# Kernel optimization log

Measured on AMD Instinct MI355X. Metric: run time of the kernel, lower is better.

## Reference

```python
import jax, jax.numpy as jnp
import numpy as np

N = 20000
E = 320000
H = 16
C = 16
NUM_GRAPHS = 64
NEG_SLOPE = 0.2


def _gat(x, edge_index, W, a_src, a_dst, bias):
    # PyG GATConv, concat=True, shared lin for src/dst, eval mode (no dropout)
    h = (x @ W).reshape(-1, H, C)                       # [N,H,C]
    src, dst = edge_index[0], edge_index[1]
    alpha_src = jnp.sum(h * a_src, axis=-1)             # [N,H]
    alpha_dst = jnp.sum(h * a_dst, axis=-1)             # [N,H]
    alpha = alpha_src[src] + alpha_dst[dst]             # [E,H]
    alpha = jax.nn.leaky_relu(alpha, NEG_SLOPE)
    amax = jax.ops.segment_max(alpha, dst, num_segments=N)
    ex = jnp.exp(alpha - amax[dst])
    denom = jax.ops.segment_sum(ex, dst, num_segments=N)
    attn = ex / jnp.where(denom == 0, 1.0, denom)[dst]  # [E,H]
    msg = h[src] * attn[:, :, None]                     # [E,H,C]
    out = jax.ops.segment_sum(msg, dst, num_segments=N) # [N,H,C]
    return out.reshape(-1, H * C) + bias


def setup_inputs() -> dict:
    key = jax.random.key(0)
    ks = jax.random.split(key, 32)
    d = {}
    d['x'] = jax.random.normal(ks[0], (N, 20), dtype=jnp.float32)
    d['edge_index_ipv6'] = jax.random.randint(ks[1], (2, E), 0, N)
    d['edge_attr_ipv6'] = jax.random.normal(ks[2], (E, 19), dtype=jnp.float32)
    d['edge_index_tsch'] = jax.random.randint(ks[3], (2, E), 0, N)
    d['edge_attr_tsch'] = jax.random.normal(ks[4], (E, 7), dtype=jnp.float32)
    d['batch'] = jnp.sort(jax.random.randint(ks[5], (N,), 0, NUM_GRAPHS))
    s = 0.1
    d['W_i'] = jax.random.normal(ks[6], (20, H * C), dtype=jnp.float32) * s
    d['a_src_i'] = jax.random.normal(ks[7], (H, C), dtype=jnp.float32) * s
    d['a_dst_i'] = jax.random.normal(ks[8], (H, C), dtype=jnp.float32) * s
    d['b_i'] = jnp.zeros((H * C,), dtype=jnp.float32)
    d['W_t'] = jax.random.normal(ks[9], (20, H * C), dtype=jnp.float32) * s
    d['a_src_t'] = jax.random.normal(ks[10], (H, C), dtype=jnp.float32) * s
    d['a_dst_t'] = jax.random.normal(ks[11], (H, C), dtype=jnp.float32) * s
    d['b_t'] = jnp.zeros((H * C,), dtype=jnp.float32)
    d['Wf'] = jax.random.normal(ks[12], (512, 64), dtype=jnp.float32) * s
    d['bf'] = jnp.zeros((64,), dtype=jnp.float32)
    d['W1'] = jax.random.normal(ks[13], (64, 32), dtype=jnp.float32) * s
    d['b1'] = jnp.zeros((32,), dtype=jnp.float32)
    d['W2'] = jax.random.normal(ks[14], (32, 16), dtype=jnp.float32) * s
    d['b2'] = jnp.zeros((16,), dtype=jnp.float32)
    d['W3'] = jax.random.normal(ks[15], (16, 16), dtype=jnp.float32) * s
    d['b3'] = jnp.zeros((16,), dtype=jnp.float32)
    d['Wce'] = jax.random.normal(ks[16], (16, 3), dtype=jnp.float32) * s
    d['bce'] = jnp.zeros((3,), dtype=jnp.float32)
    d['Wcv'] = jax.random.normal(ks[17], (16, 3), dtype=jnp.float32) * s
    d['bcv'] = jnp.zeros((3,), dtype=jnp.float32)
    return d


def reference(x, edge_index_ipv6, edge_attr_ipv6, edge_index_tsch, edge_attr_tsch,
              batch, W_i, a_src_i, a_dst_i, b_i, W_t, a_src_t, a_dst_t, b_t,
              Wf, bf, W1, b1, W2, b2, W3, b3, Wce, bce, Wcv, bcv):
    # edge_attr_* are ignored by GATConv (edge_dim=None in PyG), as in original
    n_ipv6 = _gat(x, edge_index_ipv6, W_i, a_src_i, a_dst_i, b_i)
    n_tsch = _gat(x, edge_index_tsch, W_t, a_src_t, a_dst_t, b_t)
    h = jnp.concatenate([n_ipv6, n_tsch], axis=-1)      # [N,512]
    h = jax.nn.relu(h @ Wf + bf)
    h = jax.nn.relu(h @ W1 + b1)
    h = jax.nn.relu(h @ W2 + b2)
    h = jax.nn.relu(h @ W3 + b3)                        # [N,16]
    ssum = jax.ops.segment_sum(h, batch, num_segments=NUM_GRAPHS)
    cnt = jax.ops.segment_sum(jnp.ones((h.shape[0], 1), h.dtype), batch,
                              num_segments=NUM_GRAPHS)
    g = ssum / jnp.where(cnt == 0, 1.0, cnt)            # [G,16]
    out_event = g @ Wce + bce
    out_env = g @ Wcv + bcv
    return out_event, out_env
```

## Files before the change

kernel.cpp:

```cpp
#include <hip/hip_runtime.h>
#include <math.h>

#define N_NODES 20000
#define N_EDGES 320000
#define NG 64
#define NEG 0.2f
#define NCHUNK ((N_NODES + 255) / 256)
#define FLAGBIT (1 << 30)

typedef __attribute__((ext_vector_type(8))) short bf16x8;
typedef __attribute__((ext_vector_type(4))) float f32x4;

__device__ __forceinline__ unsigned short f2bf(float f) {
  unsigned int u = __float_as_uint(f);
  return (unsigned short)((u + 0x7fffu + ((u >> 16) & 1u)) >> 16);
}
__device__ __forceinline__ unsigned int pk2bf(float a, float b) {
  return (unsigned int)f2bf(a) | ((unsigned int)f2bf(b) << 16);
}

__global__ __launch_bounds__(256) void k_front(
    const float* __restrict__ x,
    const float* __restrict__ W_i, const float* __restrict__ as_i, const float* __restrict__ ad_i,
    const float* __restrict__ W_t, const float* __restrict__ as_t, const float* __restrict__ ad_t,
    const float* __restrict__ Wf, const float* __restrict__ bf,
    const float* __restrict__ b_i, const float* __restrict__ b_t,
    const int* __restrict__ ei0, const int* __restrict__ ei1,
    unsigned short* __restrict__ wbigfrag, float* __restrict__ bfold,
    unsigned short* __restrict__ xpadbf,
    float* __restrict__ asrc0, float* __restrict__ adst0,
    float* __restrict__ asrc1, float* __restrict__ adst1,
    int* __restrict__ fill0, int* __restrict__ fill1) {
  __shared__ float bred[4][64];
  __shared__ float xs[16][20];
  __shared__ float ws[20][64];
  int b = blockIdx.x, t = threadIdx.x;
  if (b < 160) {
    int idx = b * 256 + t;
    int ct = idx / 10240, rem = idx % 10240;
    int lane = (rem >> 3) & 63, j = rem & 7, ks = rem >> 9;
    int k = ks * 32 + ((lane >> 4) << 3) + j;
    int nc = ct * 16 + (lane & 15);
    int g = (k >= 320) ? 1 : 0;
    int r = k - g * 320;
    int ch = r >> 4, h = r & 15;
    float v = 0.f;
    if (ch < 20) {
      const float* W = g ? W_t : W_i;
      const float* wr = W + ch * 256 + (h << 4);
      const float* wf = Wf + ((g << 8) + (h << 4)) * 64 + nc;
#pragma unroll
      for (int m = 0; m < 16; ++m) v = fmaf(wr[m], wf[m * 64], v);
    }
    wbigfrag[idx] = f2bf(v);
    return;
  }
  if (b == 160) {
    int wv = t >> 6, j = t & 63;
    float p = 0.f;
    int i0 = wv * 128;
#pragma unroll 4
    for (int i = i0; i < i0 + 128; ++i) {
      float bb = (i < 256) ? b_i[i] : b_t[i - 256];
      p = fmaf(bb, Wf[i * 64 + j], p);
    }
    bred[wv][j] = p;
    __syncthreads();
    if (wv == 0) bfold[j] = bred[0][j] + bred[1][j] + bred[2][j] + bred[3][j] + bf[j];
    return;
  }
  int a = b - 161;
  int e = a * 256 + t;
  int d0 = ei0[N_EDGES + e];
  int d1 = ei1[N_EDGES + e];
  atomicAdd(&fill0[d0], 1);
  atomicAdd(&fill1[d1], 1);
  int n0 = a * 16;
  for (int i = t; i < 320; i += 256) {
    int nd = i / 20, k = i % 20;
    xs[nd][k] = x[(n0 + nd) * 20 + k];
  }
  for (int i = t; i < 1280; i += 256) {
    int k = i >> 6, c = i & 63;
    int set = c >> 5, role = (c >> 4) & 1, h = c & 15;
    const float* W = set ? W_t : W_i;
    const float* av = set ? (role ? ad_t : as_t) : (role ? ad_i : as_i);
    float v = 0.f;
#pragma unroll
    for (int j = 0; j < 16; ++j) v = fmaf(W[k * 256 + h * 16 + j], av[h * 16 + j], v);
    ws[k][c] = v;
  }
  __syncthreads();
  for (int i = t; i < 512; i += 256) {
    int nd = i >> 5, j = i & 31;
    float v = (j < 20) ? xs[nd][j] : (j == 20 ? 1.f : 0.f);
    xpadbf[(size_t)(n0 + nd) * 32 + j] = f2bf(v);
  }
#pragma unroll
  for (int i = 0; i < 4; ++i) {
    int wi = i * 256 + t;
    int nd = wi >> 6, c = wi & 63;
    float v = 0.f;
#pragma unroll
    for (int k = 0; k < 20; ++k) v = fmaf(xs[nd][k], ws[k][c], v);
    int n = n0 + nd, h = c & 15;
    float* arr = (c >> 5) ? ((c >> 4) & 1 ? adst1 : asrc1)
                          : ((c >> 4) & 1 ? adst0 : asrc0);
    arr[n * 16 + h] = v;
  }
}

__global__ __launch_bounds__(256) void k_scan(
    int* __restrict__ fill0, int* __restrict__ fill1,
    int* __restrict__ rp0, int* __restrict__ rp1,
    int* __restrict__ aggs) {
  int chunk = blockIdx.x, set = blockIdx.y;
  int* fill = set ? fill1 : fill0;
  int* rp = set ? rp1 : rp0;
  int t = threadIdx.x, lane = t & 63, wv = t >> 6;
  int i = chunk * 256 + t;
  int v = (i < N_NODES) ? fill[i] : 0;
  int s = v;
#pragma unroll
  for (int d = 1; d < 64; d <<= 1) {
    int o = __shfl_up(s, d);
    if (lane >= d) s += o;
  }
  __shared__ int wsum[4];
  if (lane == 63) wsum[wv] = s;
  __syncthreads();
  int pre = 0;
#pragma unroll
  for (int j = 0; j < 4; ++j)
    if (j < wv) pre += wsum[j];
  s += pre;
  int agg = wsum[0] + wsum[1] + wsum[2] + wsum[3];
  if (t == 0)
    __hip_atomic_store(&aggs[set * 128 + chunk], agg | FLAGBIT,
                       __ATOMIC_RELEASE, __HIP_MEMORY_SCOPE_AGENT);
  __shared__ int reds[256];
  int part = 0;
  for (int j = t; j < chunk; j += 256) {
    int a;
    do {
      a = __hip_atomic_load(&aggs[set * 128 + j], __ATOMIC_ACQUIRE,
                            __HIP_MEMORY_SCOPE_AGENT);
    } while (!(a & FLAGBIT));
    part += a & (FLAGBIT - 1);
  }
  reds[t] = part;
  __syncthreads();
  for (int st = 128; st > 0; st >>= 1) {
    if (t < st) reds[t] += reds[t + st];
    __syncthreads();
  }
  int carry = reds[0];
  int excl = carry + s - v;
  if (i < N_NODES) {
    rp[i] = excl;
    fill[i] = excl;
    if (i == N_NODES - 1) rp[N_NODES] = excl + v;
  }
}

__global__ void k_scatter(const int* __restrict__ ei0, const int* __restrict__ ei1,
                          int* __restrict__ fill0, int* __restrict__ fill1,
                          unsigned short* __restrict__ srcs0,
                          unsigned short* __restrict__ srcs1) {
  int e = blockIdx.x * blockDim.x + threadIdx.x;
  if (e >= N_EDGES) return;
  const int* ei = blockIdx.y ? ei1 : ei0;
  int* fill = blockIdx.y ? fill1 : fill0;
  unsigned short* srcs = blockIdx.y ? srcs1 : srcs0;
  int d = ei[N_EDGES + e];
  int pos = atomicAdd(&fill[d], 1);
  srcs[pos] = (unsigned short)ei[e];
}

__global__ __launch_bounds__(256) void k_gat(
    const unsigned short* __restrict__ xpadbf,
    const float* __restrict__ asrc0, const float* __restrict__ adst0,
    const float* __restrict__ asrc1, const float* __restrict__ adst1,
    const int* __restrict__ rp0, const unsigned short* __restrict__ srcs0,
    const int* __restrict__ rp1, const unsigned short* __restrict__ srcs1,
    unsigned short* __restrict__ xagg) {
  __shared__ unsigned short exsh[4][16][40];
  __shared__ unsigned short xtsh[4][2][16][40];
  int w4 = threadIdx.x >> 6, lane = threadIdx.x & 63;
  int n = blockIdx.x * 2 + (w4 >> 1);
  int g = w4 & 1;
  int eid = lane & 15, slot = lane >> 4;
  unsigned short (*ext)[40] = exsh[w4];
  unsigned short (*xtw)[16][40] = xtsh[w4];
  const float* asrc = g ? asrc1 : asrc0;
  const float* adst = g ? adst1 : adst0;
  const int* rp = g ? rp1 : rp0;
  const unsigned short* srcs = g ? srcs1 : srcs0;
  int k0 = rp[n], k1 = rp[n + 1];
  const float4 adn4 = *(const float4*)&adst[n * 16 + slot * 4];
  f32x4 acc0 = {0.f, 0.f, 0.f, 0.f}, acc1 = acc0;
  int h16 = lane & 15, e8 = (lane >> 4) * 8;
  for (int base = k0; base < k1; base += 32) {
    int e0 = base + 2 * eid, e1 = e0 + 1;
    int sa = (int)srcs[min(e0, k1 - 1)];
    int sbb = (int)srcs[min(e1, k1 - 1)];
    const float4 ava = *(const float4*)&asrc[sa * 16 + slot * 4];
    const float4 avb = *(const float4*)&asrc[sbb * 16 + slot * 4];
    const uint4 xra = *(const uint4*)&xpadbf[(size_t)sa * 32 + slot * 8];
    const uint4 xrb = *(const uint4*)&xpadbf[(size_t)sbb * 32 + slot * 8];
    float ea[4], eb[4];
    {
      float a;
      bool v0 = e0 < k1, v1 = e1 < k1;
      a = ava.x + adn4.x; a = a >= 0.f ? a : NEG * a; ea[0] = v0 ? __expf(a) : 0.f;
      a = ava.y + adn4.y; a = a >= 0.f ? a : NEG * a; ea[1] = v0 ? __expf(a) : 0.f;
      a = ava.z + adn4.z; a = a >= 0.f ? a : NEG * a; ea[2] = v0 ? __expf(a) : 0.f;
      a = ava.w + adn4.w; a = a >= 0.f ? a : NEG * a; ea[3] = v0 ? __expf(a) : 0.f;
      a = avb.x + adn4.x; a = a >= 0.f ? a : NEG * a; eb[0] = v1 ? __expf(a) : 0.f;
      a = avb.y + adn4.y; a = a >= 0.f ? a : NEG * a; eb[1] = v1 ? __expf(a) : 0.f;
      a = avb.z + adn4.z; a = a >= 0.f ? a : NEG * a; eb[2] = v1 ? __expf(a) : 0.f;
      a = avb.w + adn4.w; a = a >= 0.f ? a : NEG * a; eb[3] = v1 ? __expf(a) : 0.f;
    }
#pragma unroll
    for (int r = 0; r < 4; ++r)
      *(unsigned int*)&ext[slot * 4 + r][2 * eid] = pk2bf(ea[r], eb[r]);
    unsigned int ua[4] = {xra.x, xra.y, xra.z, xra.w};
    unsigned int ub[4] = {xrb.x, xrb.y, xrb.z, xrb.w};
#pragma unroll
    for (int q = 0; q < 8; ++q) {
      unsigned int baq = (q & 1) ? (ua[q >> 1] >> 16) : (ua[q >> 1] & 0xffffu);
      unsigned int bbq = (q & 1) ? (ub[q >> 1] >> 16) : (ub[q >> 1] & 0xffffu);
      int ch = slot * 8 + q;
      *(unsigned int*)&xtw[ch >> 4][ch & 15][2 * eid] = baq | (bbq << 16);
    }
    bf16x8 A = *(const bf16x8*)&ext[h16][e8];
    bf16x8 B0 = *(const bf16x8*)&xtw[0][h16][e8];
    bf16x8 B1 = *(const bf16x8*)&xtw[1][h16][e8];
    acc0 = __builtin_amdgcn_mfma_f32_16x16x32_bf16(A, B0, acc0, 0, 0, 0);
    acc1 = __builtin_amdgcn_mfma_f32_16x16x32_bf16(A, B1, acc1, 0, 0, 0);
  }
  float inv[4];
#pragma unroll
  for (int r = 0; r < 4; ++r) {
    float dr = __shfl(acc1[r], (lane & 48) | 4);
    inv[r] = dr > 0.f ? 1.f / dr : 0.f;
  }
  int s = lane >> 4, c = lane & 15;
  size_t nb = (size_t)n * 640 + g * 320;
  uint2 o0;
  o0.x = pk2bf(acc0[0] * inv[0], acc0[1] * inv[1]);
  o0.y = pk2bf(acc0[2] * inv[2], acc0[3] * inv[3]);
  *(uint2*)&xagg[nb + c * 16 + s * 4] = o0;
  if (c < 4) {
    uint2 o1;
    o1.x = pk2bf(acc1[0] * inv[0], acc1[1] * inv[1]);
    o1.y = pk2bf(acc1[2] * inv[2], acc1[3] * inv[3]);
    *(uint2*)&xagg[nb + 256 + c * 16 + s * 4] = o1;
  }
}

__global__ __launch_bounds__(256) void k_mlp(
    const unsigned short* __restrict__ xagg, const unsigned short* __restrict__ wbigfrag,
    const float* __restrict__ bfold,
    const float* __restrict__ W1m, const float* __restrict__ b1v,
    const float* __restrict__ W2m, const float* __restrict__ b2v,
    const float* __restrict__ W3m, const float* __restrict__ b3v,
    const int* __restrict__ batch,
    float* __restrict__ gsum, int* __restrict__ gcnt) {
  int t = threadIdx.x, w = t >> 6, lane = t & 63;
  int n0 = blockIdx.x * 16;
  __shared__ float o1[16][68];
  __shared__ float o2[16][36];
  __shared__ float o3[16][20];
  __shared__ float o4[16][17];
  __shared__ int bs[16];
  if (t < 16) bs[t] = batch[n0 + t];

  {
    int m = lane & 15, kb = lane >> 4;
    const unsigned short* aptr = xagg + (size_t)(n0 + m) * 640 + kb * 8;
    const unsigned short* bbase = wbigfrag + (size_t)w * 10240 + lane * 8;
    f32x4 acc = {0.f, 0.f, 0.f, 0.f};
#pragma unroll 5
    for (int ks = 0; ks < 20; ++ks) {
      bf16x8 af = *(const bf16x8*)(aptr + ks * 32);
      bf16x8 bfr = *(const bf16x8*)(bbase + (size_t)ks * 512);
      acc = __builtin_amdgcn_mfma_f32_16x16x32_bf16(af, bfr, acc, 0, 0, 0);
    }
    int col = lane & 15, rg = lane >> 4;
#pragma unroll
    for (int r = 0; r < 4; ++r) {
      int row = rg * 4 + r;
      o1[row][w * 16 + col] = fmaxf(acc[r] + bfold[w * 16 + col], 0.f);
    }
  }
  __syncthreads();
  int nd = t >> 4, js = t & 15;
  {
    float a0 = b1v[js], a1 = b1v[js + 16];
#pragma unroll 8
    for (int k = 0; k < 64; ++k) {
      float hv = o1[nd][k];
      a0 = fmaf(hv, W1m[k * 32 + js], a0);
      a1 = fmaf(hv, W1m[k * 32 + js + 16], a1);
    }
    o2[nd][js] = fmaxf(a0, 0.f);
    o2[nd][js + 16] = fmaxf(a1, 0.f);
  }
  __syncthreads();
  {
    float a = b2v[js];
#pragma unroll
    for (int k = 0; k < 32; ++k) a = fmaf(o2[nd][k], W2m[k * 16 + js], a);
    o3[nd][js] = fmaxf(a, 0.f);
  }
  __syncthreads();
  {
    float a = b3v[js];
#pragma unroll
    for (int k = 0; k < 16; ++k) a = fmaf(o3[nd][k], W3m[k * 16 + js], a);
    o4[nd][js] = fmaxf(a, 0.f);
  }
  __syncthreads();
  if (t < 128) {
    int s = t >> 4, jx = t & 15;
    int b = bs[0] + s;
    if (b <= bs[15]) {
      float sum = 0.f; int c = 0;
#pragma unroll
      for (int ndd = 0; ndd < 16; ++ndd)
        if (bs[ndd] == b) { sum += o4[ndd][jx]; ++c; }
      if (c > 0) {
        atomicAdd(&gsum[b * 16 + jx], sum);
        if (jx == 0) atomicAdd(&gcnt[b], c);
      }
    }
  }
}

__global__ void k_head(const float* __restrict__ gsum, const int* __restrict__ gcnt,
                       const float* __restrict__ Wce, const float* __restrict__ bce,
                       const float* __restrict__ Wcv, const float* __restrict__ bcv,
                       float* __restrict__ out) {
  int t = threadIdx.x;
  if (t >= 384) return;
  int half = t / 192, idx = t % 192;
  int b = idx / 3, r = idx % 3;
  float cnt = (float)gcnt[b];
  float inv = cnt > 0.f ? 1.f / cnt : 1.f;
  const float* Wc = half ? Wcv : Wce;
  const float* bc = half ? bcv : bce;
  float v = bc[r];
#pragma unroll
  for (int j = 0; j < 16; ++j) v = fmaf(gsum[b * 16 + j] * inv, Wc[j * 3 + r], v);
  out[t] = v;
}

extern "C" void kernel_launch(void* const* d_in, const int* in_sizes, int n_in,
                              void* d_out, int out_size, void* d_ws, size_t ws_size,
                              hipStream_t stream) {
  const float* x = (const float*)d_in[0];
  const int* ei_i = (const int*)d_in[1];
  const int* ei_t = (const int*)d_in[3];
  const int* batch = (const int*)d_in[5];
  const float* W_i = (const float*)d_in[6];
  const float* as_i = (const float*)d_in[7];
  const float* ad_i = (const float*)d_in[8];
  const float* b_i = (const float*)d_in[9];
  const float* W_t = (const float*)d_in[10];
  const float* as_t = (const float*)d_in[11];
  const float* ad_t = (const float*)d_in[12];
  const float* b_t = (const float*)d_in[13];
  const float* Wf = (const float*)d_in[14];
  const float* bf = (const float*)d_in[15];
  const float* W1 = (const float*)d_in[16];
  const float* b1 = (const float*)d_in[17];
  const float* W2 = (const float*)d_in[18];
  const float* b2 = (const float*)d_in[19];
  const float* W3 = (const float*)d_in[20];
  const float* b3 = (const float*)d_in[21];
  const float* Wce = (const float*)d_in[22];
  const float* bce = (const float*)d_in[23];
  const float* Wcv = (const float*)d_in[24];
  const float* bcv = (const float*)d_in[25];

  char* ws = (char*)d_ws;
  size_t off = 0;
  auto take = [&](size_t bytes) {
    void* p = ws + off;
    off = (off + bytes + 255) & ~(size_t)255;
    return p;
  };
  unsigned short* xpadbf = (unsigned short*)take((size_t)N_NODES * 32 * 2);
  unsigned short* xagg = (unsigned short*)take((size_t)N_NODES * 640 * 2);
  unsigned short* wbigfrag = (unsigned short*)take((size_t)40960 * 2);
  float* bfold = (float*)take((size_t)64 * 4);
  float* asrc_i = (float*)take((size_t)N_NODES * 16 * 4);
  float* adst_i = (float*)take((size_t)N_NODES * 16 * 4);
  float* asrc_t = (float*)take((size_t)N_NODES * 16 * 4);
  float* adst_t = (float*)take((size_t)N_NODES * 16 * 4);
  int* rowptr_i = (int*)take((size_t)(N_NODES + 1) * 4);
  int* rowptr_t = (int*)take((size_t)(N_NODES + 1) * 4);
  int* fill_i = (int*)take((size_t)2 * N_NODES * 4);
  int* fill_t = fill_i + N_NODES;
  unsigned short* srcs_i = (unsigned short*)take((size_t)N_EDGES * 2);
  unsigned short* srcs_t = (unsigned short*)take((size_t)N_EDGES * 2);
  float* gsum = (float*)take((size_t)(NG * 16 + NG + 256) * 4);
  int* gcnt = (int*)(gsum + NG * 16);
  int* csums = gcnt + NG;

  hipMemsetAsync(fill_i, 0, (size_t)2 * N_NODES * 4, stream);
  hipMemsetAsync(gsum, 0, (size_t)(NG * 16 + NG + 256) * 4, stream);

  k_front<<<1411, 256, 0, stream>>>(x, W_i, as_i, ad_i, W_t, as_t, ad_t,
                                    Wf, bf, b_i, b_t, ei_i, ei_t,
                                    wbigfrag, bfold, xpadbf,
                                    asrc_i, adst_i, asrc_t, adst_t,
                                    fill_i, fill_t);

  dim3 sgrid(NCHUNK, 2);
  k_scan<<<sgrid, 256, 0, stream>>>(fill_i, fill_t, rowptr_i, rowptr_t, csums);

  dim3 egrid((N_EDGES + 255) / 256, 2);
  k_scatter<<<egrid, 256, 0, stream>>>(ei_i, ei_t, fill_i, fill_t, srcs_i, srcs_t);

  k_gat<<<N_NODES / 2, 256, 0, stream>>>(xpadbf, asrc_i, adst_i, asrc_t, adst_t,
                                         rowptr_i, srcs_i, rowptr_t, srcs_t,
                                         xagg);

  k_mlp<<<N_NODES / 16, 256, 0, stream>>>(xagg, wbigfrag, bfold,
                                          W1, b1, W2, b2, W3, b3,
                                          batch, gsum, gcnt);

  k_head<<<1, 384, 0, stream>>>(gsum, gcnt, Wce, bce, Wcv, bcv, (float*)d_out);
}
```

Measured before the change: 137.8 us.

## Fuse all stages into one cooperative persistent kernel with grid syncs

Replaces the six separate kernel launches with a single persistent cooperative kernel. Each former kernel becomes a grid-strided phase, separated by grid.sync(), and the two memsets are merged into one. This removes per-launch overhead and inter-kernel gaps. In exchange, occupancy is capped by the cooperative grid size, five grid-wide barriers are added, and the GAT and MLP phases now loop over virtual blocks instead of oversubscribing the GPU. hipGetDeviceProperties and the occupancy query also run on the host on every call.

```diff
diff --git a/kernel.cpp b/kernel.cpp
--- a/kernel.cpp
+++ b/kernel.cpp
@@ -1,5 +1,8 @@
 #include <hip/hip_runtime.h>
+#include <hip/hip_cooperative_groups.h>
 #include <math.h>
+
+namespace cg = cooperative_groups;
 
 #define N_NODES 20000
 #define N_EDGES 320000
@@ -19,371 +22,344 @@
   return (unsigned int)f2bf(a) | ((unsigned int)f2bf(b) << 16);
 }
 
-__global__ __launch_bounds__(256) void k_front(
-    const float* __restrict__ x,
-    const float* __restrict__ W_i, const float* __restrict__ as_i, const float* __restrict__ ad_i,
-    const float* __restrict__ W_t, const float* __restrict__ as_t, const float* __restrict__ ad_t,
-    const float* __restrict__ Wf, const float* __restrict__ bf,
-    const float* __restrict__ b_i, const float* __restrict__ b_t,
-    const int* __restrict__ ei0, const int* __restrict__ ei1,
-    unsigned short* __restrict__ wbigfrag, float* __restrict__ bfold,
-    unsigned short* __restrict__ xpadbf,
-    float* __restrict__ asrc0, float* __restrict__ adst0,
-    float* __restrict__ asrc1, float* __restrict__ adst1,
-    int* __restrict__ fill0, int* __restrict__ fill1) {
-  __shared__ float bred[4][64];
-  __shared__ float xs[16][20];
-  __shared__ float ws[20][64];
-  int b = blockIdx.x, t = threadIdx.x;
-  if (b < 160) {
-    int idx = b * 256 + t;
-    int ct = idx / 10240, rem = idx % 10240;
-    int lane = (rem >> 3) & 63, j = rem & 7, ks = rem >> 9;
-    int k = ks * 32 + ((lane >> 4) << 3) + j;
-    int nc = ct * 16 + (lane & 15);
-    int g = (k >= 320) ? 1 : 0;
-    int r = k - g * 320;
-    int ch = r >> 4, h = r & 15;
-    float v = 0.f;
-    if (ch < 20) {
-      const float* W = g ? W_t : W_i;
-      const float* wr = W + ch * 256 + (h << 4);
-      const float* wf = Wf + ((g << 8) + (h << 4)) * 64 + nc;
-#pragma unroll
-      for (int m = 0; m < 16; ++m) v = fmaf(wr[m], wf[m * 64], v);
-    }
-    wbigfrag[idx] = f2bf(v);
-    return;
-  }
-  if (b == 160) {
-    int wv = t >> 6, j = t & 63;
-    float p = 0.f;
-    int i0 = wv * 128;
+struct KParams {
+  const float* x;
+  const int* ei_i; const int* ei_t; const int* batch;
+  const float *W_i, *as_i, *ad_i, *b_i;
+  const float *W_t, *as_t, *ad_t, *b_t;
+  const float *Wf, *bf, *W1, *b1, *W2, *b2, *W3, *b3;
+  const float *Wce, *bce, *Wcv, *bcv;
+  unsigned short* xpadbf; unsigned short* xagg; unsigned short* wbigfrag;
+  float* bfold;
+  float *asrc_i, *adst_i, *asrc_t, *adst_t;
+  int *rowptr_i, *rowptr_t, *fill_i, *fill_t, *csums;
+  unsigned short *srcs_i, *srcs_t;
+  float* gsum; int* gcnt; float* out;
+};
+
+__global__ __launch_bounds__(256, 4) void k_mega(KParams P) {
+  cg::grid_group grid = cg::this_grid();
+  __shared__ __align__(16) char smem_[15360];
+  int t = threadIdx.x;
+  int nb = gridDim.x;
+
+  {
+    float* xs = (float*)smem_;
+    float* wsA = (float*)(smem_ + 1280);
+    float* bred = (float*)(smem_ + 6400);
+    for (int vb = blockIdx.x; vb < 1411; vb += nb) {
+      if (vb < 160) {
+        int idx = vb * 256 + t;
+        int ct = idx / 10240, rem = idx % 10240;
+        int lane = (rem >> 3) & 63, j = rem & 7, ks = rem >> 9;
+        int k = ks * 32 + ((lane >> 4) << 3) + j;
+        int nc = ct * 16 + (lane & 15);
+        int g = (k >= 320) ? 1 : 0;
+        int r = k - g * 320;
+        int ch = r >> 4, h = r & 15;
+        float v = 0.f;
+        if (ch < 20) {
+          const float* W = g ? P.W_t : P.W_i;
+          const float* wr = W + ch * 256 + (h << 4);
+          const float* wf = P.Wf + ((g << 8) + (h << 4)) * 64 + nc;
+#pragma unroll
+          for (int m = 0; m < 16; ++m) v = fmaf(wr[m], wf[m * 64], v);
+        }
+        P.wbigfrag[idx] = f2bf(v);
+      } else if (vb == 160) {
+        int wv = t >> 6, j = t & 63;
+        float pp = 0.f;
+        int i0 = wv * 128;
 #pragma unroll 4
-    for (int i = i0; i < i0 + 128; ++i) {
-      float bb = (i < 256) ? b_i[i] : b_t[i - 256];
-      p = fmaf(bb, Wf[i * 64 + j], p);
-    }
-    bred[wv][j] = p;
+        for (int i = i0; i < i0 + 128; ++i) {
+          float bb = (i < 256) ? P.b_i[i] : P.b_t[i - 256];
+          pp = fmaf(bb, P.Wf[i * 64 + j], pp);
+        }
+        bred[wv * 64 + j] = pp;
+        __syncthreads();
+        if (wv == 0)
+          P.bfold[j] = bred[j] + bred[64 + j] + bred[128 + j] + bred[192 + j] + P.bf[j];
+      } else {
+        int a = vb - 161;
+        int e = a * 256 + t;
+        atomicAdd(&P.fill_i[P.ei_i[N_EDGES + e]], 1);
+        atomicAdd(&P.fill_t[P.ei_t[N_EDGES + e]], 1);
+        int n0 = a * 16;
+        for (int i = t; i < 320; i += 256) {
+          int nd = i / 20, k = i % 20;
+          xs[nd * 20 + k] = P.x[(n0 + nd) * 20 + k];
+        }
+        for (int i = t; i < 1280; i += 256) {
+          int k = i >> 6, c = i & 63;
+          int set = c >> 5, role = (c >> 4) & 1, h = c & 15;
+          const float* W = set ? P.W_t : P.W_i;
+          const float* av = set ? (role ? P.ad_t : P.as_t) : (role ? P.ad_i : P.as_i);
+          float v = 0.f;
+#pragma unroll
+          for (int j = 0; j < 16; ++j) v = fmaf(W[k * 256 + h * 16 + j], av[h * 16 + j], v);
+          wsA[k * 64 + c] = v;
+        }
+        __syncthreads();
+        for (int i = t; i < 512; i += 256) {
+          int nd = i >> 5, j = i & 31;
+          float v = (j < 20) ? xs[nd * 20 + j] : (j == 20 ? 1.f : 0.f);
+          P.xpadbf[(size_t)(n0 + nd) * 32 + j] = f2bf(v);
+        }
+#pragma unroll
+        for (int i = 0; i < 4; ++i) {
+          int wi = i * 256 + t;
+          int nd = wi >> 6, c = wi & 63;
+          float v = 0.f;
+#pragma unroll
+          for (int k = 0; k < 20; ++k) v = fmaf(xs[nd * 20 + k], wsA[k * 64 + c], v);
+          int n = n0 + nd, h = c & 15;
+          float* arr = (c >> 5) ? ((c >> 4) & 1 ? P.adst_t : P.asrc_t)
+                                : ((c >> 4) & 1 ? P.adst_i : P.asrc_i);
+          arr[n * 16 + h] = v;
+        }
+      }
+      __syncthreads();
+    }
+  }
+  grid.sync();
+
+  if (blockIdx.x < 2 * NCHUNK) {
+    int* wsum = (int*)smem_;
+    int* reds = (int*)smem_ + 4;
+    int chunk = blockIdx.x % NCHUNK, set = blockIdx.x / NCHUNK;
+    int* fill = set ? P.fill_t : P.fill_i;
+    int* rp = set ? P.rowptr_t : P.rowptr_i;
+    int lane = t & 63, wv = t >> 6;
+    int i = chunk * 256 + t;
+    int v = (i < N_NODES) ? fill[i] : 0;
+    int s = v;
+#pragma unroll
+    for (int d = 1; d < 64; d <<= 1) {
+      int o = __shfl_up(s, d);
+      if (lane >= d) s += o;
+    }
+    if (lane == 63) wsum[wv] = s;
     __syncthreads();
-    if (wv == 0) bfold[j] = bred[0][j] + bred[1][j] + bred[2][j] + bred[3][j] + bf[j];
-    return;
-  }
-  int a = b - 161;
-  int e = a * 256 + t;
-  int d0 = ei0[N_EDGES + e];
-  int d1 = ei1[N_EDGES + e];
-  atomicAdd(&fill0[d0], 1);
-  atomicAdd(&fill1[d1], 1);
-  int n0 = a * 16;
-  for (int i = t; i < 320; i += 256) {
-    int nd = i / 20, k = i % 20;
-    xs[nd][k] = x[(n0 + nd) * 20 + k];
-  }
-  for (int i = t; i < 1280; i += 256) {
-    int k = i >> 6, c = i & 63;
-    int set = c >> 5, role = (c >> 4) & 1, h = c & 15;
-    const float* W = set ? W_t : W_i;
-    const float* av = set ? (role ? ad_t : as_t) : (role ? ad_i : as_i);
-    float v = 0.f;
-#pragma unroll
-    for (int j = 0; j < 16; ++j) v = fmaf(W[k * 256 + h * 16 + j], av[h * 16 + j], v);
-    ws[k][c] = v;
-  }
-  __syncthreads();
-  for (int i = t; i < 512; i += 256) {
-    int nd = i >> 5, j = i & 31;
-    float v = (j < 20) ? xs[nd][j] : (j == 20 ? 1.f : 0.f);
-    xpadbf[(size_t)(n0 + nd) * 32 + j] = f2bf(v);
-  }
-#pragma unroll
-  for (int i = 0; i < 4; ++i) {
-    int wi = i * 256 + t;
-    int nd = wi >> 6, c = wi & 63;
-    float v = 0.f;
-#pragma unroll
-    for (int k = 0; k < 20; ++k) v = fmaf(xs[nd][k], ws[k][c], v);
-    int n = n0 + nd, h = c & 15;
-    float* arr = (c >> 5) ? ((c >> 4) & 1 ? adst1 : asrc1)
-                          : ((c >> 4) & 1 ? adst0 : asrc0);
-    arr[n * 16 + h] = v;
-  }
-}
-
-__global__ __launch_bounds__(256) void k_scan(
-    int* __restrict__ fill0, int* __restrict__ fill1,
-    int* __restrict__ rp0, int* __restrict__ rp1,
-    int* __restrict__ aggs) {
-  int chunk = blockIdx.x, set = blockIdx.y;
-  int* fill = set ? fill1 : fill0;
-  int* rp = set ? rp1 : rp0;
-  int t = threadIdx.x, lane = t & 63, wv = t >> 6;
-  int i = chunk * 256 + t;
-  int v = (i < N_NODES) ? fill[i] : 0;
-  int s = v;
-#pragma unroll
-  for (int d = 1; d < 64; d <<= 1) {
-    int o = __shfl_up(s, d);
-    if (lane >= d) s += o;
-  }
-  __shared__ int wsum[4];
-  if (lane == 63) wsum[wv] = s;
-  __syncthreads();
-  int pre = 0;
-#pragma unroll
-  for (int j = 0; j < 4; ++j)
-    if (j < wv) pre += wsum[j];
-  s += pre;
-  int agg = wsum[0] + wsum[1] + wsum[2] + wsum[3];
-  if (t == 0)
-    __hip_atomic_store(&aggs[set * 128 + chunk], agg | FLAGBIT,
-                       __ATOMIC_RELEASE, __HIP_MEMORY_SCOPE_AGENT);
-  __shared__ int reds[256];
-  int part = 0;
-  for (int j = t; j < chunk; j += 256) {
-    int a;
-    do {
-      a = __hip_atomic_load(&aggs[set * 128 + j], __ATOMIC_ACQUIRE,
-                            __HIP_MEMORY_SCOPE_AGENT);
-    } while (!(a & FLAGBIT));
-    part += a & (FLAGBIT - 1);
-  }
-  reds[t] = part;
-  __syncthreads();
-  for (int st = 128; st > 0; st >>= 1) {
-    if (t < st) reds[t] += reds[t + st];
+    int pre = 0;
+#pragma unroll
+    for (int j = 0; j < 4; ++j)
+      if (j < wv) pre += wsum[j];
+    s += pre;
+    int agg = wsum[0] + wsum[1] + wsum[2] + wsum[3];
+    if (t == 0)
+      __hip_atomic_store(&P.csums[set * 128 + chunk], agg | FLAGBIT,
+                         __ATOMIC_RELEASE, __HIP_MEMORY_SCOPE_AGENT);
+    int part = 0;
+    for (int j = t; j < chunk; j += 256) {
+      int a;
+      do {
+        a = __hip_atomic_load(&P.csums[set * 128 + j], __ATOMIC_ACQUIRE,
+                              __HIP_MEMORY_SCOPE_AGENT);
+      } while (!(a & FLAGBIT));
+      part += a & (FLAGBIT - 1);
+    }
+    reds[t] = part;
     __syncthreads();
-  }
-  int carry = reds[0];
-  int excl = carry + s - v;
-  if (i < N_NODES) {
-    rp[i] = excl;
-    fill[i] = excl;
-    if (i == N_NODES - 1) rp[N_NODES] = excl + v;
-  }
-}
-
-__global__ void k_scatter(const int* __restrict__ ei0, const int* __restrict__ ei1,
-                          int* __restrict__ fill0, int* __restrict__ fill1,
-                          unsigned short* __restrict__ srcs0,
-                          unsigned short* __restrict__ srcs1) {
-  int e = blockIdx.x * blockDim.x + threadIdx.x;
-  if (e >= N_EDGES) return;
-  const int* ei = blockIdx.y ? ei1 : ei0;
-  int* fill = blockIdx.y ? fill1 : fill0;
-  unsigned short* srcs = blockIdx.y ? srcs1 : srcs0;
-  int d = ei[N_EDGES + e];
-  int pos = atomicAdd(&fill[d], 1);
-  srcs[pos] = (unsigned short)ei[e];
-}
-
-__global__ __launch_bounds__(256) void k_gat(
-    const unsigned short* __restrict__ xpadbf,
-    const float* __restrict__ asrc0, const float* __restrict__ adst0,
-    const float* __restrict__ asrc1, const float* __restrict__ adst1,
-    const int* __restrict__ rp0, const unsigned short* __restrict__ srcs0,
-    const int* __restrict__ rp1, const unsigned short* __restrict__ srcs1,
-    unsigned short* __restrict__ xagg) {
-  __shared__ unsigned short exsh[4][16][40];
-  __shared__ unsigned short xtsh[4][2][16][40];
-  int w4 = threadIdx.x >> 6, lane = threadIdx.x & 63;
-  int n = blockIdx.x * 2 + (w4 >> 1);
-  int g = w4 & 1;
-  int eid = lane & 15, slot = lane >> 4;
-  unsigned short (*ext)[40] = exsh[w4];
-  unsigned short (*xtw)[16][40] = xtsh[w4];
-  const float* asrc = g ? asrc1 : asrc0;
-  const float* adst = g ? adst1 : adst0;
-  const int* rp = g ? rp1 : rp0;
-  const unsigned short* srcs = g ? srcs1 : srcs0;
-  int k0 = rp[n], k1 = rp[n + 1];
-  const float4 adn4 = *(const float4*)&adst[n * 16 + slot * 4];
-  f32x4 acc0 = {0.f, 0.f, 0.f, 0.f}, acc1 = acc0;
-  int h16 = lane & 15, e8 = (lane >> 4) * 8;
-  for (int base = k0; base < k1; base += 32) {
-    int e0 = base + 2 * eid, e1 = e0 + 1;
-    int sa = (int)srcs[min(e0, k1 - 1)];
-    int sbb = (int)srcs[min(e1, k1 - 1)];
-    const float4 ava = *(const float4*)&asrc[sa * 16 + slot * 4];
-    const float4 avb = *(const float4*)&asrc[sbb * 16 + slot * 4];
-    const uint4 xra = *(const uint4*)&xpadbf[(size_t)sa * 32 + slot * 8];
-    const uint4 xrb = *(const uint4*)&xpadbf[(size_t)sbb * 32 + slot * 8];
-    float ea[4], eb[4];
-    {
-      float a;
-      bool v0 = e0 < k1, v1 = e1 < k1;
-      a = ava.x + adn4.x; a = a >= 0.f ? a : NEG * a; ea[0] = v0 ? __expf(a) : 0.f;
-      a = ava.y + adn4.y; a = a >= 0.f ? a : NEG * a; ea[1] = v0 ? __expf(a) : 0.f;
-      a = ava.z + adn4.z; a = a >= 0.f ? a : NEG * a; ea[2] = v0 ? __expf(a) : 0.f;
-      a = ava.w + adn4.w; a = a >= 0.f ? a : NEG * a; ea[3] = v0 ? __expf(a) : 0.f;
-      a = avb.x + adn4.x; a = a >= 0.f ? a : NEG * a; eb[0] = v1 ? __expf(a) : 0.f;
-      a = avb.y + adn4.y; a = a >= 0.f ? a : NEG * a; eb[1] = v1 ? __expf(a) : 0.f;
-      a = avb.z + adn4.z; a = a >= 0.f ? a : NEG * a; eb[2] = v1 ? __expf(a) : 0.f;
-      a = avb.w + adn4.w; a = a >= 0.f ? a : NEG * a; eb[3] = v1 ? __expf(a) : 0.f;
-    }
-#pragma unroll
-    for (int r = 0; r < 4; ++r)
-      *(unsigned int*)&ext[slot * 4 + r][2 * eid] = pk2bf(ea[r], eb[r]);
-    unsigned int ua[4] = {xra.x, xra.y, xra.z, xra.w};
-    unsigned int ub[4] = {xrb.x, xrb.y, xrb.z, xrb.w};
-#pragma unroll
-    for (int q = 0; q < 8; ++q) {
-      unsigned int baq = (q & 1) ? (ua[q >> 1] >> 16) : (ua[q >> 1] & 0xffffu);
-      unsigned int bbq = (q & 1) ? (ub[q >> 1] >> 16) : (ub[q >> 1] & 0xffffu);
-      int ch = slot * 8 + q;
-      *(unsigned int*)&xtw[ch >> 4][ch & 15][2 * eid] = baq | (bbq << 16);
-    }
-    bf16x8 A = *(const bf16x8*)&ext[h16][e8];
-    bf16x8 B0 = *(const bf16x8*)&xtw[0][h16][e8];
-    bf16x8 B1 = *(const bf16x8*)&xtw[1][h16][e8];
-    acc0 = __builtin_amdgcn_mfma_f32_16x16x32_bf16(A, B0, acc0, 0, 0, 0);
-    acc1 = __builtin_amdgcn_mfma_f32_16x16x32_bf16(A, B1, acc1, 0, 0, 0);
-  }
-  float inv[4];
-#pragma unroll
-  for (int r = 0; r < 4; ++r) {
-    float dr = __shfl(acc1[r], (lane & 48) | 4);
-    inv[r] = dr > 0.f ? 1.f / dr : 0.f;
-  }
-  int s = lane >> 4, c = lane & 15;
-  size_t nb = (size_t)n * 640 + g * 320;
-  uint2 o0;
-  o0.x = pk2bf(acc0[0] * inv[0], acc0[1] * inv[1]);
-  o0.y = pk2bf(acc0[2] * inv[2], acc0[3] * inv[3]);
-  *(uint2*)&xagg[nb + c * 16 + s * 4] = o0;
-  if (c < 4) {
-    uint2 o1;
-    o1.x = pk2bf(acc1[0] * inv[0], acc1[1] * inv[1]);
-    o1.y = pk2bf(acc1[2] * inv[2], acc1[3] * inv[3]);
-    *(uint2*)&xagg[nb + 256 + c * 16 + s * 4] = o1;
-  }
-}
-
-__global__ __launch_bounds__(256) void k_mlp(
-    const unsigned short* __restrict__ xagg, const unsigned short* __restrict__ wbigfrag,
-    const float* __restrict__ bfold,
-    const float* __restrict__ W1m, const float* __restrict__ b1v,
-    const float* __restrict__ W2m, const float* __restrict__ b2v,
-    const float* __restrict__ W3m, const float* __restrict__ b3v,
-    const int* __restrict__ batch,
-    float* __restrict__ gsum, int* __restrict__ gcnt) {
-  int t = threadIdx.x, w = t >> 6, lane = t & 63;
-  int n0 = blockIdx.x * 16;
-  __shared__ float o1[16][68];
-  __shared__ float o2[16][36];
-  __shared__ float o3[16][20];
-  __shared__ float o4[16][17];
-  __shared__ int bs[16];
-  if (t < 16) bs[t] = batch[n0 + t];
+    for (int st = 128; st > 0; st >>= 1) {
+      if (t < st) reds[t] += reds[t + st];
+      __syncthreads();
+    }
+    int carry = reds[0];
+    int excl = carry + s - v;
+    if (i < N_NODES) {
+      rp[i] = excl;
+      fill[i] = excl;
+      if (i == N_NODES - 1) rp[N_NODES] = excl + v;
+    }
+  }
+  grid.sync();
+
+  for (int vb = blockIdx.x; vb < 2 * 1250; vb += nb) {
+    int set = vb >= 1250;
+    int e = (vb - set * 1250) * 256 + t;
+    const int* ei = set ? P.ei_t : P.ei_i;
+    int* fill = set ? P.fill_t : P.fill_i;
+    unsigned short* srcs = set ? P.srcs_t : P.srcs_i;
+    int d = ei[N_EDGES + e];
+    int pos = atomicAdd(&fill[d], 1);
+    srcs[pos] = (unsigned short)ei[e];
+  }
+  grid.sync();
 
   {
-    int m = lane & 15, kb = lane >> 4;
-    const unsigned short* aptr = xagg + (size_t)(n0 + m) * 640 + kb * 8;
-    const unsigned short* bbase = wbigfrag + (size_t)w * 10240 + lane * 8;
-    f32x4 acc = {0.f, 0.f, 0.f, 0.f};
+    int w4 = t >> 6, lane = t & 63;
+    int eid = lane & 15, slot = lane >> 4;
+    int h16 = lane & 15, e8 = (lane >> 4) * 8;
+    unsigned short* ext = (unsigned short*)smem_ + w4 * 640;
+    unsigned short* xtw = (unsigned short*)(smem_ + 5120) + w4 * 1280;
+    for (int vb = blockIdx.x; vb < N_NODES / 2; vb += nb) {
+      int n = vb * 2 + (w4 >> 1);
+      int g = w4 & 1;
+      const float* asrc = g ? P.asrc_t : P.asrc_i;
+      const float* adst = g ? P.adst_t : P.adst_i;
+      const int* rp = g ? P.rowptr_t : P.rowptr_i;
+      const unsigned short* srcs = g ? P.srcs_t : P.srcs_i;
+      int k0 = rp[n], k1 = rp[n + 1];
+      const float4 adn4 = *(const float4*)&adst[n * 16 + slot * 4];
+      f32x4 acc0 = {0.f, 0.f, 0.f, 0.f}, acc1 = acc0;
+      for (int base = k0; base < k1; base += 32) {
+        int e0 = base + 2 * eid, e1 = e0 + 1;
+        int sa = (int)srcs[min(e0, k1 - 1)];
+        int sbb = (int)srcs[min(e1, k1 - 1)];
+        const float4 ava = *(const float4*)&asrc[sa * 16 + slot * 4];
+        const float4 avb = *(const float4*)&asrc[sbb * 16 + slot * 4];
+        const uint4 xra = *(const uint4*)&P.xpadbf[(size_t)sa * 32 + slot * 8];
+        const uint4 xrb = *(const uint4*)&P.xpadbf[(size_t)sbb * 32 + slot * 8];
+        float ea[4], eb[4];
+        {
+          float a;
+          bool v0 = e0 < k1, v1 = e1 < k1;
+          a = ava.x + adn4.x; a = a >= 0.f ? a : NEG * a; ea[0] = v0 ? __expf(a) : 0.f;
+          a = ava.y + adn4.y; a = a >= 0.f ? a : NEG * a; ea[1] = v0 ? __expf(a) : 0.f;
+          a = ava.z + adn4.z; a = a >= 0.f ? a : NEG * a; ea[2] = v0 ? __expf(a) : 0.f;
+          a = ava.w + adn4.w; a = a >= 0.f ? a : NEG * a; ea[3] = v0 ? __expf(a) : 0.f;
+          a = avb.x + adn4.x; a = a >= 0.f ? a : NEG * a; eb[0] = v1 ? __expf(a) : 0.f;
+          a = avb.y + adn4.y; a = a >= 0.f ? a : NEG * a; eb[1] = v1 ? __expf(a) : 0.f;
+          a = avb.z + adn4.z; a = a >= 0.f ? a : NEG * a; eb[2] = v1 ? __expf(a) : 0.f;
+          a = avb.w + adn4.w; a = a >= 0.f ? a : NEG * a; eb[3] = v1 ? __expf(a) : 0.f;
+        }
+#pragma unroll
+        for (int r = 0; r < 4; ++r)
+          *(unsigned int*)&ext[(slot * 4 + r) * 40 + 2 * eid] = pk2bf(ea[r], eb[r]);
+        unsigned int ua[4] = {xra.x, xra.y, xra.z, xra.w};
+        unsigned int ub[4] = {xrb.x, xrb.y, xrb.z, xrb.w};
+#pragma unroll
+        for (int q = 0; q < 8; ++q) {
+          unsigned int baq = (q & 1) ? (ua[q >> 1] >> 16) : (ua[q >> 1] & 0xffffu);
+          unsigned int bbq = (q & 1) ? (ub[q >> 1] >> 16) : (ub[q >> 1] & 0xffffu);
+          int ch = slot * 8 + q;
+          *(unsigned int*)&xtw[(ch >> 4) * 640 + (ch & 15) * 40 + 2 * eid] =
+              baq | (bbq << 16);
+        }
+        bf16x8 A = *(const bf16x8*)&ext[h16 * 40 + e8];
+        bf16x8 B0 = *(const bf16x8*)&xtw[h16 * 40 + e8];
+        bf16x8 B1 = *(const bf16x8*)&xtw[640 + h16 * 40 + e8];
+        acc0 = __builtin_amdgcn_mfma_f32_16x16x32_bf16(A, B0, acc0, 0, 0, 0);
+        acc1 = __builtin_amdgcn_mfma_f32_16x16x32_bf16(A, B1, acc1, 0, 0, 0);
+      }
+      float inv[4];
+#pragma unroll
+      for (int r = 0; r < 4; ++r) {
+        float dr = __shfl(acc1[r], (lane & 48) | 4);
+        inv[r] = dr > 0.f ? 1.f / dr : 0.f;
+      }
+      int ss = lane >> 4, c = lane & 15;
+      size_t nbase = (size_t)n * 640 + g * 320;
+      uint2 o0;
+      o0.x = pk2bf(acc0[0] * inv[0], acc0[1] * inv[1]);
+      o0.y = pk2bf(acc0[2] * inv[2], acc0[3] * inv[3]);
+      *(uint2*)&P.xagg[nbase + c * 16 + ss * 4] = o0;
+      if (c < 4) {
+        uint2 o1v;
+        o1v.x = pk2bf(acc1[0] * inv[0], acc1[1] * inv[1]);
+        o1v.y = pk2bf(acc1[2] * inv[2], acc1[3] * inv[3]);
+        *(uint2*)&P.xagg[nbase + 256 + c * 16 + ss * 4] = o1v;
+      }
+    }
+  }
+  grid.sync();
+
+  {
+    float* o1 = (float*)smem_;
+    float* o2 = o1 + 1088;
+    float* o3 = o2 + 576;
+    float* o4 = o3 + 320;
+    int* bs = (int*)(o4 + 272);
+    int w = t >> 6, lane = t & 63;
+    for (int vb = blockIdx.x; vb < N_NODES / 16; vb += nb) {
+      int n0 = vb * 16;
+      if (t < 16) bs[t] = P.batch[n0 + t];
+      {
+        int m = lane & 15, kb = lane >> 4;
+        const unsigned short* aptr = P.xagg + (size_t)(n0 + m) * 640 + kb * 8;
+        const unsigned short* bbase = P.wbigfrag + (size_t)w * 10240 + lane * 8;
+        f32x4 acc = {0.f, 0.f, 0.f, 0.f};
 #pragma unroll 5
-    for (int ks = 0; ks < 20; ++ks) {
-      bf16x8 af = *(const bf16x8*)(aptr + ks * 32);
-      bf16x8 bfr = *(const bf16x8*)(bbase + (size_t)ks * 512);
-      acc = __builtin_amdgcn_mfma_f32_16x16x32_bf16(af, bfr, acc, 0, 0, 0);
-    }
-    int col = lane & 15, rg = lane >> 4;
-#pragma unroll
-    for (int r = 0; r < 4; ++r) {
-      int row = rg * 4 + r;
-      o1[row][w * 16 + col] = fmaxf(acc[r] + bfold[w * 16 + col], 0.f);
-    }
-  }
-  __syncthreads();
-  int nd = t >> 4, js = t & 15;
-  {
-    float a0 = b1v[js], a1 = b1v[js + 16];
+        for (int ks = 0; ks < 20; ++ks) {
+          bf16x8 af = *(const bf16x8*)(aptr + ks * 32);
+          bf16x8 bfr = *(const bf16x8*)(bbase + (size_t)ks * 512);
+          acc = __builtin_amdgcn_mfma_f32_16x16x32_bf16(af, bfr, acc, 0, 0, 0);
+        }
+        int col = lane & 15, rg = lane >> 4;
+#pragma unroll
+        for (int r = 0; r < 4; ++r) {
+          int row = rg * 4 + r;
+          o1[row * 68 + w * 16 + col] =
+              fmaxf(acc[r] + P.bfold[w * 16 + col], 0.f);
+        }
+      }
+      __syncthreads();
+      int nd = t >> 4, js = t & 15;
+      {
+        float a0 = P.b1[js], a1 = P.b1[js + 16];
 #pragma unroll 8
-    for (int k = 0; k < 64; ++k) {
-      float hv = o1[nd][k];
-      a0 = fmaf(hv, W1m[k * 32 + js], a0);
-      a1 = fmaf(hv, W1m[k * 32 + js + 16], a1);
-    }
-    o2[nd][js] = fmaxf(a0, 0.f);
-    o2[nd][js + 16] = fmaxf(a1, 0.f);
-  }
-  __syncthreads();
-  {
-    float a = b2v[js];
-#pragma unroll
-    for (int k = 0; k < 32; ++k) a = fmaf(o2[nd][k], W2m[k * 16 + js], a);
-    o3[nd][js] = fmaxf(a, 0.f);
-  }
-  __syncthreads();
-  {
-    float a = b3v[js];
-#pragma unroll
-    for (int k = 0; k < 16; ++k) a = fmaf(o3[nd][k], W3m[k * 16 + js], a);
-    o4[nd][js] = fmaxf(a, 0.f);
-  }
-  __syncthreads();
-  if (t < 128) {
-    int s = t >> 4, jx = t & 15;
-    int b = bs[0] + s;
-    if (b <= bs[15]) {
-      float sum = 0.f; int c = 0;
-#pragma unroll
-      for (int ndd = 0; ndd < 16; ++ndd)
-        if (bs[ndd] == b) { sum += o4[ndd][jx]; ++c; }
-      if (c > 0) {
-        atomicAdd(&gsum[b * 16 + jx], sum);
-        if (jx == 0) atomicAdd(&gcnt[b], c);
-      }
-    }
-  }
-}
-
-__global__ void k_head(const float* __restrict__ gsum, const int* __restrict__ gcnt,
-                       const float* __restrict__ Wce, const float* __restrict__ bce,
-                       const float* __restrict__ Wcv, const float* __restrict__ bcv,
-                       float* __restrict__ out) {
-  int t = threadIdx.x;
-  if (t >= 384) return;
-  int half = t / 192, idx = t % 192;
-  int b = idx / 3, r = idx % 3;
-  float cnt = (float)gcnt[b];
-  float inv = cnt > 0.f ? 1.f / cnt : 1.f;
-  const float* Wc = half ? Wcv : Wce;
-  const float* bc = half ? bcv : bce;
-  float v = bc[r];
-#pragma unroll
-  for (int j = 0; j < 16; ++j) v = fmaf(gsum[b * 16 + j] * inv, Wc[j * 3 + r], v);
-  out[t] = v;
+        for (int k = 0; k < 64; ++k) {
+          float hv = o1[nd * 68 + k];
+          a0 = fmaf(hv, P.W1[k * 32 + js], a0);
+          a1 = fmaf(hv, P.W1[k * 32 + js + 16], a1);
+        }
+        o2[nd * 36 + js] = fmaxf(a0, 0.f);
+        o2[nd * 36 + js + 16] = fmaxf(a1, 0.f);
+      }
+      __syncthreads();
+      {
+        float a = P.b2[js];
+#pragma unroll
+        for (int k = 0; k < 32; ++k) a = fmaf(o2[nd * 36 + k], P.W2[k * 16 + js], a);
+        o3[nd * 20 + js] = fmaxf(a, 0.f);
+      }
+      __syncthreads();
+      {
+        float a = P.b3[js];
+#pragma unroll
+        for (int k = 0; k < 16; ++k) a = fmaf(o3[nd * 20 + k], P.W3[k * 16 + js], a);
+        o4[nd * 17 + js] = fmaxf(a, 0.f);
+      }
+      __syncthreads();
+      if (t < 128) {
+        int s = t >> 4, jx = t & 15;
+        int b = bs[0] + s;
+        if (b <= bs[15]) {
+          float sum = 0.f;
+          int c = 0;
+#pragma unroll
+          for (int ndd = 0; ndd < 16; ++ndd)
+            if (bs[ndd] == b) { sum += o4[ndd * 17 + jx]; ++c; }
+          if (c > 0) {
+            atomicAdd(&P.gsum[b * 16 + jx], sum);
+            if (jx == 0) atomicAdd(&P.gcnt[b], c);
+          }
+        }
+      }
+      __syncthreads();
+    }
+  }
+  grid.sync();
+
+  if (blockIdx.x == 0) {
+    for (int o = t; o < 384; o += 256) {
+      int half = o / 192, idx = o % 192;
+      int b = idx / 3, r = idx % 3;
+      float cnt = (float)P.gcnt[b];
+      float inv = cnt > 0.f ? 1.f / cnt : 1.f;
+      const float* Wc = half ? P.Wcv : P.Wce;
+      const float* bc = half ? P.bcv : P.bce;
+      float v = bc[r];
+#pragma unroll
+      for (int j = 0; j < 16; ++j) v = fmaf(P.gsum[b * 16 + j] * inv, Wc[j * 3 + r], v);
+      P.out[o] = v;
+    }
+  }
 }
 
 extern "C" void kernel_launch(void* const* d_in, const int* in_sizes, int n_in,
                               void* d_out, int out_size, void* d_ws, size_t ws_size,
                               hipStream_t stream) {
-  const float* x = (const float*)d_in[0];
-  const int* ei_i = (const int*)d_in[1];
-  const int* ei_t = (const int*)d_in[3];
-  const int* batch = (const int*)d_in[5];
-  const float* W_i = (const float*)d_in[6];
-  const float* as_i = (const float*)d_in[7];
-  const float* ad_i = (const float*)d_in[8];
-  const float* b_i = (const float*)d_in[9];
-  const float* W_t = (const float*)d_in[10];
-  const float* as_t = (const float*)d_in[11];
-  const float* ad_t = (const float*)d_in[12];
-  const float* b_t = (const float*)d_in[13];
-  const float* Wf = (const float*)d_in[14];
-  const float* bf = (const float*)d_in[15];
-  const float* W1 = (const float*)d_in[16];
-  const float* b1 = (const float*)d_in[17];
-  const float* W2 = (const float*)d_in[18];
-  const float* b2 = (const float*)d_in[19];
-  const float* W3 = (const float*)d_in[20];
-  const float* b3 = (const float*)d_in[21];
-  const float* Wce = (const float*)d_in[22];
-  const float* bce = (const float*)d_in[23];
-  const float* Wcv = (const float*)d_in[24];
-  const float* bcv = (const float*)d_in[25];
-
   char* ws = (char*)d_ws;
   size_t off = 0;
   auto take = [&](size_t bytes) {
@@ -391,46 +367,66 @@
     off = (off + bytes + 255) & ~(size_t)255;
     return p;
   };
-  unsigned short* xpadbf = (unsigned short*)take((size_t)N_NODES * 32 * 2);
-  unsigned short* xagg = (unsigned short*)take((size_t)N_NODES * 640 * 2);
-  unsigned short* wbigfrag = (unsigned short*)take((size_t)40960 * 2);
-  float* bfold = (float*)take((size_t)64 * 4);
-  float* asrc_i = (float*)take((size_t)N_NODES * 16 * 4);
-  float* adst_i = (float*)take((size_t)N_NODES * 16 * 4);
-  float* asrc_t = (float*)take((size_t)N_NODES * 16 * 4);
-  float* adst_t = (float*)take((size_t)N_NODES * 16 * 4);
-  int* rowptr_i = (int*)take((size_t)(N_NODES + 1) * 4);
-  int* rowptr_t = (int*)take((size_t)(N_NODES + 1) * 4);
-  int* fill_i = (int*)take((size_t)2 * N_NODES * 4);
-  int* fill_t = fill_i + N_NODES;
-  unsigned short* srcs_i = (unsigned short*)take((size_t)N_EDGES * 2);
-  unsigned short* srcs_t = (unsigned short*)take((size_t)N_EDGES * 2);
-  float* gsum = (float*)take((size_t)(NG * 16 + NG + 256) * 4);
-  int* gcnt = (int*)(gsum + NG * 16);
-  int* csums = gcnt + NG;
-
-  hipMemsetAsync(fill_i, 0, (size_t)2 * N_NODES * 4, stream);
-  hipMemsetAsync(gsum, 0, (size_t)(NG * 16 + NG + 256) * 4, stream);
-
-  k_front<<<1411, 256, 0, stream>>>(x, W_i, as_i, ad_i, W_t, as_t, ad_t,
-                                    Wf, bf, b_i, b_t, ei_i, ei_t,
-                                    wbigfrag, bfold, xpadbf,
-                                    asrc_i, adst_i, asrc_t, adst_t,
-                                    fill_i, fill_t);
-
-  dim3 sgrid(NCHUNK, 2);
-  k_scan<<<sgrid, 256, 0, stream>>>(fill_i, fill_t, rowptr_i, rowptr_t, csums);
-
-  dim3 egrid((N_EDGES + 255) / 256, 2);
-  k_scatter<<<egrid, 256, 0, stream>>>(ei_i, ei_t, fill_i, fill_t, srcs_i, srcs_t);
-
-  k_gat<<<N_NODES / 2, 256, 0, stream>>>(xpadbf, asrc_i, adst_i, asrc_t, adst_t,
-                                         rowptr_i, srcs_i, rowptr_t, srcs_t,
-                                         xagg);
-
-  k_mlp<<<N_NODES / 16, 256, 0, stream>>>(xagg, wbigfrag, bfold,
-                                          W1, b1, W2, b2, W3, b3,
-                                          batch, gsum, gcnt);
-
-  k_head<<<1, 384, 0, stream>>>(gsum, gcnt, Wce, bce, Wcv, bcv, (float*)d_out);
+  KParams P;
+  P.x = (const float*)d_in[0];
+  P.ei_i = (const int*)d_in[1];
+  P.ei_t = (const int*)d_in[3];
+  P.batch = (const int*)d_in[5];
+  P.W_i = (const float*)d_in[6];
+  P.as_i = (const float*)d_in[7];
+  P.ad_i = (const float*)d_in[8];
+  P.b_i = (const float*)d_in[9];
+  P.W_t = (const float*)d_in[10];
+  P.as_t = (const float*)d_in[11];
+  P.ad_t = (const float*)d_in[12];
+  P.b_t = (const float*)d_in[13];
+  P.Wf = (const float*)d_in[14];
+  P.bf = (const float*)d_in[15];
+  P.W1 = (const float*)d_in[16];
+  P.b1 = (const float*)d_in[17];
+  P.W2 = (const float*)d_in[18];
+  P.b2 = (const float*)d_in[19];
+  P.W3 = (const float*)d_in[20];
+  P.b3 = (const float*)d_in[21];
+  P.Wce = (const float*)d_in[22];
+  P.bce = (const float*)d_in[23];
+  P.Wcv = (const float*)d_in[24];
+  P.bcv = (const float*)d_in[25];
+
+  P.xpadbf = (unsigned short*)take((size_t)N_NODES * 32 * 2);
+  P.xagg = (unsigned short*)take((size_t)N_NODES * 640 * 2);
+  P.wbigfrag = (unsigned short*)take((size_t)40960 * 2);
+  P.bfold = (float*)take((size_t)64 * 4);
+  P.asrc_i = (float*)take((size_t)N_NODES * 16 * 4);
+  P.adst_i = (float*)take((size_t)N_NODES * 16 * 4);
+  P.asrc_t = (float*)take((size_t)N_NODES * 16 * 4);
+  P.adst_t = (float*)take((size_t)N_NODES * 16 * 4);
+  P.rowptr_i = (int*)take((size_t)(N_NODES + 1) * 4);
+  P.rowptr_t = (int*)take((size_t)(N_NODES + 1) * 4);
+  P.srcs_i = (unsigned short*)take((size_t)N_EDGES * 2);
+  P.srcs_t = (unsigned short*)take((size_t)N_EDGES * 2);
+  int zero_ints = N_NODES + N_NODES + NG * 16 + NG + 256;
+  P.fill_i = (int*)take((size_t)zero_ints * 4);
+  P.fill_t = P.fill_i + N_NODES;
+  P.gsum = (float*)(P.fill_t + N_NODES);
+  P.gcnt = (int*)(P.gsum + NG * 16);
+  P.csums = P.gcnt + NG;
+  P.out = (float*)d_out;
+
+  hipMemsetAsync(P.fill_i, 0, (size_t)zero_ints * 4, stream);
+
+  int occ = 0;
+  hipOccupancyMaxActiveBlocksPerMultiprocessor(&occ, k_mega, 256, 0);
+  if (occ < 1) occ = 1;
+  int numCU = 256;
+  hipDeviceProp_t prop;
+  int dev = 0;
+  if (hipGetDevice(&dev) == hipSuccess &&
+      hipGetDeviceProperties(&prop, dev) == hipSuccess)
+    numCU = prop.multiProcessorCount;
+  int grid = numCU * occ;
+  if (grid < 2 * NCHUNK) grid = 2 * NCHUNK;
+
+  void* args[] = {(void*)&P};
+  hipLaunchCooperativeKernel(k_mega, dim3(grid), dim3(256), args, 0, stream);
 }
```

Measured after the change: 454.6 us. 230% more time.
